# Kernel tuning notes

Hardware: AMD Instinct MI355X
Metric: run time of the kernel (lower is better)

Reference implementation:

```python
import jax, jax.numpy as jnp
import numpy as np

VOCAB, H, B, S = 30522, 768, 32, 512


def setup_inputs() -> dict:
    key = jax.random.key(0)
    ks = jax.random.split(key, 12)
    inp = {
        'hiddens': jax.random.normal(ks[0], (B, S, H), dtype=jnp.float32),
        'input_ids': jax.random.randint(ks[1], (B, S), 0, VOCAB, dtype=jnp.int32),
        'in_table': jax.random.bernoulli(ks[2], 0.5, (VOCAB,)),
        'table': jax.random.normal(ks[3], (VOCAB, H), dtype=jnp.float32) * 0.05,
        'W1m': jax.random.normal(ks[4], (512, H), dtype=jnp.float32) * 0.03,
        'b1m': jnp.zeros((512,), jnp.float32),
        'W2m': jax.random.normal(ks[5], (H, 512), dtype=jnp.float32) * 0.03,
        'b2m': jnp.zeros((H,), jnp.float32),
        'Wa1': jax.random.normal(ks[6], (100, H), dtype=jnp.float32) * 0.03,
        'ba1': jnp.zeros((100,), jnp.float32),
        'Wa2': jax.random.normal(ks[7], (1, 100), dtype=jnp.float32) * 0.1,
        'ba2': jnp.zeros((1,), jnp.float32),
        'Wl': jax.random.normal(ks[8], (3, 2 * H), dtype=jnp.float32) * 0.02,
        'bl': jnp.zeros((3,), jnp.float32),
    }
    return inp


def reference(hiddens, input_ids, in_table, table, W1m, b1m, W2m, b2m,
              Wa1, ba1, Wa2, ba2, Wl, bl):
    # --- vectorized replacement of the per-token dict lookup + MLP2 loops ---
    # gather knowledge vectors for every token: [B,S,768]
    know = table[input_ids]
    # MLP2 up to X2 (only X2 is used downstream): 768 -> 512 -> 768, relu twice
    x = jax.nn.relu(jnp.einsum('bsh,kh->bsk', know, W1m) + b1m)   # [B,S,512]
    fine = jax.nn.relu(jnp.einsum('bsk,hk->bsh', x, W2m) + b2m)   # [B,S,768]
    # membership mask; position 0 (CLS) is never looked up in the loop
    pos = jnp.arange(input_ids.shape[1])[None, :]                 # [1,S]
    mask = in_table[input_ids] & (pos > 0)                        # [B,S] bool
    m = mask[..., None].astype(hiddens.dtype)
    # wordhiddens: fine vector where token in table else zeros
    wordhiddens = fine * m                                        # [B,S,768]
    # --- StructuredSelfAttention over wordhiddens[:, 1:] ---
    wh = wordhiddens[:, 1:]                                       # [B,S-1,768]
    a = jnp.tanh(jnp.einsum('bsh,ah->bsa', wh, Wa1) + ba1)        # [B,S-1,100]
    a = jnp.einsum('bsa,oa->bso', a, Wa2) + ba2                   # [B,S-1,1]
    attn = jax.nn.softmax(a, axis=1)                              # softmax over seq
    sent = jnp.einsum('bso,bsh->boh', attn, wh)                   # [B,1,768]
    cls_knowledge = jnp.sum(sent, axis=1)                         # r=1, [B,768]
    # --- classifier head (method='ce'; dropout in eval mode = identity) ---
    cls_feats = jnp.concatenate([hiddens[:, 0, :], cls_knowledge], axis=1)  # [B,1536]
    predicts = cls_feats @ Wl.T + bl                              # [B,3]
    return predicts
```

## Files before the change

kernel.cpp:

```cpp
#include <hip/hip_runtime.h>
#include <stdint.h>
#include <math.h>

#define B_ 32
#define S_ 512
#define H_ 768
#define V_ 30522
#define M_ (B_*S_)
#define N1_ 512

typedef __attribute__((ext_vector_type(8))) short bf16x8;
typedef __attribute__((ext_vector_type(4))) float f32x4;

__device__ __forceinline__ float bf2f(unsigned short u){
  union { unsigned int u; float f; } c; c.u = ((unsigned int)u)<<16; return c.f;
}
__device__ __forceinline__ unsigned short f2bf(float f){
  union { float f; unsigned int u; } c; c.f=f;
  unsigned int u = c.u + 0x7FFFu + ((c.u>>16)&1u);
  return (unsigned short)(u>>16);
}
__device__ __forceinline__ bool tbl_get(const void* t, int id, int flag){
  if(flag==1) return ((const int*)t)[id]!=0;
  if(flag==2) return ((const unsigned int*)t)[id]!=0u;
  return ((const unsigned char*)t)[id]!=0;
}
__device__ __forceinline__ void gload_lds16(const void* g, void* l){
  __builtin_amdgcn_global_load_lds(
    (const __attribute__((address_space(1))) void*)g,
    (__attribute__((address_space(3))) void*)l, 16, 0, 0);
}

__global__ __launch_bounds__(256) void k_prep(const void* __restrict__ in_table,
  const int* __restrict__ ids,
  const float* __restrict__ W1, const float* __restrict__ W2,
  const float* __restrict__ Wa1, const float* __restrict__ Wa2, const float* __restrict__ ba1,
  unsigned short* __restrict__ W1bf, unsigned short* __restrict__ W2bf,
  unsigned short* __restrict__ Wa1bf, float* __restrict__ Wa2p, float* __restrict__ ba1p,
  int* __restrict__ cid, int* __restrict__ cnt)
{
  const int blk = blockIdx.x;
  const int t = threadIdx.x;
  if(blk < 32){
    __shared__ int sh[512];
    __shared__ int sflag;
    if(t < 64){
      const int v = ((const int*)in_table)[t];
      const unsigned int u = (unsigned int)v;
      const unsigned long long b01 = __ballot(v==0 || v==1);
      const unsigned long long bfl = __ballot(u==0u || u==0x3F800000u);
      if(t==0) sflag = (~b01==0ull) ? 1 : ((~bfl==0ull) ? 2 : 0);
    }
    __syncthreads();
    const int flag = sflag;
    const int m0 = blk*S_ + t, m1 = m0 + 256;
    const int id0 = ids[m0], id1 = ids[m1];
    const int mk0 = ((t!=0) && tbl_get(in_table, id0, flag)) ? 1 : 0;
    const int mk1 = tbl_get(in_table, id1, flag) ? 1 : 0;
    sh[t] = mk0; sh[t+256] = mk1;
    __syncthreads();
    for(int off=1; off<512; off<<=1){
      const int a0 = (t >= off) ? sh[t-off] : 0;
      const int a1 = (t+256 >= off) ? sh[t+256-off] : 0;
      __syncthreads();
      sh[t] += a0; sh[t+256] += a1;
      __syncthreads();
    }
    const int total = sh[511];
    const int r0 = sh[t] - mk0;
    const int r1 = sh[t+256] - mk1;
    if(t >= total)     cid[blk*S_ + t]       = 0;
    if(t+256 >= total) cid[blk*S_ + t + 256] = 0;
    if(mk0) cid[blk*S_ + r0] = id0;
    if(mk1) cid[blk*S_ + r1] = id1;
    if(t==0) cnt[blk] = total;
  } else {
    const int g = (blk-32)*256 + t, st = (gridDim.x-32)*256;
    for(int i=g;i<512*H_;i+=st) W1bf[i]=f2bf(W1[i]);
    for(int i=g;i<H_*512;i+=st) W2bf[i]=f2bf(W2[i]);
    for(int i=g;i<128*H_;i+=st) Wa1bf[i] = (i<100*H_)? f2bf(Wa1[i]) : (unsigned short)0;
    if(g < 128){ Wa2p[g] = (g<100)? Wa2[g] : 0.f; ba1p[g] = (g<100)? ba1[g] : 0.f; }
  }
}

__global__ __launch_bounds__(256) void k_gemm1g(
  const float* __restrict__ table, const int* __restrict__ cid,
  const unsigned short* __restrict__ Bw, const float* __restrict__ bias,
  const int* __restrict__ cnt, unsigned short* __restrict__ C)
{
  const int m0 = blockIdx.x << 7;
  if((m0 & (S_-1)) >= cnt[m0 >> 9]) return;
  __shared__ __align__(16) float AsF[128*32];
  __shared__ __align__(16) unsigned short Bs[128*32];
  const int tid = threadIdx.x;
  const int lane = tid & 63;
  const int wave = tid >> 6;
  const int wr = wave >> 1, wc = wave & 1;
  const int n0 = blockIdx.y << 7;

  const float* gaq[4];
  #pragma unroll
  for(int q=0;q<4;q++){
    const int s = q*256 + tid;
    const int row = s >> 3, ch = s & 7;
    const int sch = ch ^ (row & 7);
    gaq[q] = table + (size_t)cid[m0 + row]*H_ + (sch<<2);
  }
  const int f0 = tid, f1 = 256 + tid;
  const int r0 = f0 >> 2, s0 = ((f0 & 3) ^ ((f0 >> 3) & 3)) << 3;
  const int r1 = f1 >> 2, s1 = ((f1 & 3) ^ ((f1 >> 3) & 3)) << 3;
  const unsigned short* gb0 = Bw + (size_t)(n0 + r0)*H_ + s0;
  const unsigned short* gb1 = Bw + (size_t)(n0 + r1)*H_ + s1;

  f32x4 acc[4][4] = {};
  const int arow = (wr<<6) + (lane & 15);
  const int brow = (wc<<6) + (lane & 15);
  const int kg = lane >> 4;
  const int slb = ((kg ^ ((lane>>1)&3)) << 3);

  for(int k0 = 0; k0 < H_; k0 += 32){
    #pragma unroll
    for(int q=0;q<4;q++)
      gload_lds16(gaq[q] + k0, AsF + (q*256 + tid)*4);
    gload_lds16(gb0 + k0, Bs + (wave<<9));
    gload_lds16(gb1 + k0, Bs + 2048 + (wave<<9));
    __syncthreads();
    bf16x8 a[4], b[4];
    #pragma unroll
    for(int m=0;m<4;m++){
      const int R = arow + (m<<4);
      const int c1 = (2*kg) ^ (R&7), c2 = (2*kg+1) ^ (R&7);
      const f32x4 fa = *(const f32x4*)(AsF + R*32 + (c1<<2));
      const f32x4 fb = *(const f32x4*)(AsF + R*32 + (c2<<2));
      union { float f; unsigned int u; } z0,z1,z2,z3,z4,z5,z6,z7;
      z0.f=fa.x; z1.f=fa.y; z2.f=fa.z; z3.f=fa.w;
      z4.f=fb.x; z5.f=fb.y; z6.f=fb.z; z7.f=fb.w;
      union { unsigned int w[4]; bf16x8 v; } cv;
      cv.w[0] = (z1.u & 0xFFFF0000u) | (z0.u >> 16);
      cv.w[1] = (z3.u & 0xFFFF0000u) | (z2.u >> 16);
      cv.w[2] = (z5.u & 0xFFFF0000u) | (z4.u >> 16);
      cv.w[3] = (z7.u & 0xFFFF0000u) | (z6.u >> 16);
      a[m] = cv.v;
    }
    #pragma unroll
    for(int n=0;n<4;n++) b[n] = *(const bf16x8*)(Bs + (brow + (n<<4))*32 + slb);
    #pragma unroll
    for(int m=0;m<4;m++)
      #pragma unroll
      for(int n=0;n<4;n++)
        acc[m][n] = __builtin_amdgcn_mfma_f32_16x16x32_bf16(a[m], b[n], acc[m][n], 0,0,0);
    __syncthreads();
  }

  const int crow0 = (lane>>4) << 2;
  const int ccol  = lane & 15;
  float bia[4];
  #pragma unroll
  for(int n=0;n<4;n++) bia[n] = bias[n0 + (wc<<6) + (n<<4) + ccol];
  #pragma unroll
  for(int m=0;m<4;m++){
    const int gr0 = m0 + (wr<<6) + (m<<4) + crow0;
    #pragma unroll
    for(int j=0;j<4;j++){
      const size_t rbase = (size_t)(gr0 + j) * N1_;
      #pragma unroll
      for(int n=0;n<4;n++){
        float v = acc[m][n][j] + bia[n];
        v = fmaxf(v, 0.f);
        C[rbase + n0 + (wc<<6) + (n<<4) + ccol] = f2bf(v);
      }
    }
  }
}

template<int KTOT, int NTOT>
__global__ __launch_bounds__(256) void k_gemm(
  const unsigned short* __restrict__ A, const unsigned short* __restrict__ Bw,
  const float* __restrict__ bias, const int* __restrict__ cnt,
  unsigned short* __restrict__ C)
{
  const int m0 = blockIdx.x << 7;
  if((m0 & (S_-1)) >= cnt[m0 >> 9]) return;
  __shared__ __align__(16) unsigned short As[128*32];
  __shared__ __align__(16) unsigned short Bs[128*32];
  const int tid = threadIdx.x;
  const int lane = tid & 63;
  const int wave = tid >> 6;
  const int wr = wave >> 1, wc = wave & 1;
  const int n0 = blockIdx.y << 7;

  const int f0 = tid, f1 = 256 + tid;
  const int r0 = f0 >> 2, s0 = ((f0 & 3) ^ ((f0 >> 3) & 3)) << 3;
  const int r1 = f1 >> 2, s1 = ((f1 & 3) ^ ((f1 >> 3) & 3)) << 3;
  const unsigned short* ga0 = A + (size_t)(m0 + r0)*KTOT + s0;
  const unsigned short* ga1 = A + (size_t)(m0 + r1)*KTOT + s1;
  const unsigned short* gb0 = Bw + (size_t)(n0 + r0)*KTOT + s0;
  const unsigned short* gb1 = Bw + (size_t)(n0 + r1)*KTOT + s1;
  unsigned short* la0 = As + (wave<<9);
  unsigned short* la1 = As + 2048 + (wave<<9);
  unsigned short* lb0 = Bs + (wave<<9);
  unsigned short* lb1 = Bs + 2048 + (wave<<9);

  f32x4 acc[4][4] = {};
  const int arow = (wr<<6) + (lane & 15);
  const int brow = (wc<<6) + (lane & 15);
  const int sl   = (((lane>>4) ^ ((lane>>1)&3)) << 3);

  for(int k0 = 0; k0 < KTOT; k0 += 32){
    gload_lds16(ga0 + k0, la0);
    gload_lds16(ga1 + k0, la1);
    gload_lds16(gb0 + k0, lb0);
    gload_lds16(gb1 + k0, lb1);
    __syncthreads();
    bf16x8 a[4], b[4];
    #pragma unroll
    for(int m=0;m<4;m++) a[m] = *(const bf16x8*)(As + (arow + (m<<4))*32 + sl);
    #pragma unroll
    for(int n=0;n<4;n++) b[n] = *(const bf16x8*)(Bs + (brow + (n<<4))*32 + sl);
    #pragma unroll
    for(int m=0;m<4;m++)
      #pragma unroll
      for(int n=0;n<4;n++)
        acc[m][n] = __builtin_amdgcn_mfma_f32_16x16x32_bf16(a[m], b[n], acc[m][n], 0,0,0);
    __syncthreads();
  }

  const int crow0 = (lane>>4) << 2;
  const int ccol  = lane & 15;
  float bia[4];
  #pragma unroll
  for(int n=0;n<4;n++) bia[n] = bias[n0 + (wc<<6) + (n<<4) + ccol];
  #pragma unroll
  for(int m=0;m<4;m++){
    const int gr0 = m0 + (wr<<6) + (m<<4) + crow0;
    #pragma unroll
    for(int j=0;j<4;j++){
      const size_t rbase = (size_t)(gr0 + j) * NTOT;
      #pragma unroll
      for(int n=0;n<4;n++){
        float v = acc[m][n][j] + bia[n];
        v = fmaxf(v, 0.f);
        C[rbase + n0 + (wc<<6) + (n<<4) + ccol] = f2bf(v);
      }
    }
  }
}

__global__ __launch_bounds__(256) void k_score(
  const unsigned short* __restrict__ A, const unsigned short* __restrict__ Bw,
  const float* __restrict__ ba1p, const float* __restrict__ Wa2p, const float* __restrict__ ba2,
  const int* __restrict__ cnt, float* __restrict__ scoresC)
{
  const int m0 = blockIdx.x << 7;
  const int scnt = cnt[m0 >> 9];
  const int mbase = m0 & (S_-1);
  if(mbase >= scnt) return;
  __shared__ __align__(16) unsigned short As[128*32];
  __shared__ __align__(16) unsigned short Bs[128*32];
  __shared__ float sums[128][2];
  const int tid = threadIdx.x;
  const int lane = tid & 63;
  const int wave = tid >> 6;
  const int wr = wave >> 1, wc = wave & 1;

  const int f0 = tid, f1 = 256 + tid;
  const int r0 = f0 >> 2, s0 = ((f0 & 3) ^ ((f0 >> 3) & 3)) << 3;
  const int r1 = f1 >> 2, s1 = ((f1 & 3) ^ ((f1 >> 3) & 3)) << 3;
  const unsigned short* ga0 = A + (size_t)(m0 + r0)*H_ + s0;
  const unsigned short* ga1 = A + (size_t)(m0 + r1)*H_ + s1;
  const unsigned short* gb0 = Bw + (size_t)r0*H_ + s0;
  const unsigned short* gb1 = Bw + (size_t)r1*H_ + s1;
  unsigned short* la0 = As + (wave<<9);
  unsigned short* la1 = As + 2048 + (wave<<9);
  unsigned short* lb0 = Bs + (wave<<9);
  unsigned short* lb1 = Bs + 2048 + (wave<<9);

  f32x4 acc[4][4] = {};
  const int arow = (wr<<6) + (lane & 15);
  const int brow = (wc<<6) + (lane & 15);
  const int sl   = (((lane>>4) ^ ((lane>>1)&3)) << 3);

  for(int k0 = 0; k0 < H_; k0 += 32){
    gload_lds16(ga0 + k0, la0);
    gload_lds16(ga1 + k0, la1);
    gload_lds16(gb0 + k0, lb0);
    gload_lds16(gb1 + k0, lb1);
    __syncthreads();
    bf16x8 a[4], b[4];
    #pragma unroll
    for(int m=0;m<4;m++) a[m] = *(const bf16x8*)(As + (arow + (m<<4))*32 + sl);
    #pragma unroll
    for(int n=0;n<4;n++) b[n] = *(const bf16x8*)(Bs + (brow + (n<<4))*32 + sl);
    #pragma unroll
    for(int m=0;m<4;m++)
      #pragma unroll
      for(int n=0;n<4;n++)
        acc[m][n] = __builtin_amdgcn_mfma_f32_16x16x32_bf16(a[m], b[n], acc[m][n], 0,0,0);
    __syncthreads();
  }

  float psum[4][4] = {};
  #pragma unroll
  for(int n=0;n<4;n++){
    const int c = (wc<<6) + (n<<4) + (lane & 15);
    const float w2 = Wa2p[c], bb = ba1p[c];
    #pragma unroll
    for(int m=0;m<4;m++)
      #pragma unroll
      for(int j=0;j<4;j++)
        psum[m][j] = fmaf(tanhf(acc[m][n][j] + bb), w2, psum[m][j]);
  }
  #pragma unroll
  for(int msk=1; msk<16; msk<<=1)
    #pragma unroll
    for(int m=0;m<4;m++)
      #pragma unroll
      for(int j=0;j<4;j++)
        psum[m][j] += __shfl_xor(psum[m][j], msk, 64);
  if((lane & 15) == 0){
    #pragma unroll
    for(int m=0;m<4;m++)
      #pragma unroll
      for(int j=0;j<4;j++)
        sums[(wr<<6) + (m<<4) + ((lane>>4)<<2) + j][wc] = psum[m][j];
  }
  __syncthreads();
  if(tid < 128 && (mbase + tid) < scnt)
    scoresC[m0 + tid] = sums[tid][0] + sums[tid][1] + ba2[0];
}

__global__ __launch_bounds__(256) void k_partial(
  const float* __restrict__ scoresC, const int* __restrict__ cnt,
  const unsigned short* __restrict__ wh,
  const float* __restrict__ Wa2, const float* __restrict__ ba1, const float* __restrict__ ba2,
  float* __restrict__ partial)
{
  const int b = blockIdx.x >> 4, ch = blockIdx.x & 15, tid = threadIdx.x;
  const int n = cnt[b];
  const int j0 = ch << 5;
  const int nch = min(n - j0, 32);
  if(nch <= 0){
    if(tid < 192) *(float4*)(partial + (size_t)blockIdx.x*H_ + (tid<<2)) = float4{0.f,0.f,0.f,0.f};
    return;
  }
  __shared__ float red[256];
  __shared__ float sw[32];
  red[tid] = (tid < 100) ? Wa2[tid]*tanhf(ba1[tid]) : 0.f;
  __syncthreads();
  for(int st=128; st>0; st>>=1){ if(tid<st) red[tid]+=red[tid+st]; __syncthreads(); }
  const float c0 = red[0] + ba2[0];
  __syncthreads();
  const float s1 = (tid     < n) ? scoresC[b*S_ + tid      ] : -1e30f;
  const float s2 = (tid+256 < n) ? scoresC[b*S_ + tid + 256] : -1e30f;
  float lm = fmaxf(s1, s2);
  if(tid==0 && n < 511) lm = fmaxf(lm, c0);
  red[tid] = lm; __syncthreads();
  for(int st=128; st>0; st>>=1){ if(tid<st) red[tid]=fmaxf(red[tid], red[tid+st]); __syncthreads(); }
  const float mx = red[0]; __syncthreads();
  const float e1 = (tid     < n) ? __expf(s1-mx) : 0.f;
  const float e2 = (tid+256 < n) ? __expf(s2-mx) : 0.f;
  red[tid] = e1+e2; __syncthreads();
  for(int st=128; st>0; st>>=1){ if(tid<st) red[tid]+=red[tid+st]; __syncthreads(); }
  const float denom = red[0] + (float)(511 - n) * __expf(c0 - mx);
  const float inv = 1.f/denom;
  if(tid < 32){
    const int j = j0 + tid;
    sw[tid] = (j < n) ? __expf(scoresC[b*S_+j]-mx)*inv : 0.f;
  }
  __syncthreads();
  if(tid < 192){
    float a0=0.f, a1=0.f, a2=0.f, a3=0.f;
    const unsigned short* wp = wh + ((size_t)(b*S_ + j0))*H_ + (tid<<2);
    #pragma unroll 4
    for(int t=0;t<nch;t++){
      const float wv = sw[t];
      const ushort4 v = *(const ushort4*)(wp + (size_t)t*H_);
      a0 = fmaf(wv, bf2f(v.x), a0);
      a1 = fmaf(wv, bf2f(v.y), a1);
      a2 = fmaf(wv, bf2f(v.z), a2);
      a3 = fmaf(wv, bf2f(v.w), a3);
    }
    *(float4*)(partial + (size_t)blockIdx.x*H_ + (tid<<2)) = float4{a0,a1,a2,a3};
  }
}

__global__ __launch_bounds__(256) void k_predict(const float* __restrict__ hiddens,
  const float* __restrict__ partial, const float* __restrict__ Wl, const float* __restrict__ bl,
  float* __restrict__ out){
  __shared__ float ck[768];
  __shared__ float red[256];
  const int b = blockIdx.x, tid = threadIdx.x;
  #pragma unroll
  for(int r=0;r<3;r++){
    const int h = tid + (r<<8);
    float s=0.f;
    #pragma unroll 4
    for(int c=0;c<16;c++) s += partial[((size_t)((b<<4)+c))*H_ + h];
    ck[h]=s;
  }
  __syncthreads();
  const float* hid = hiddens + (size_t)b * S_ * H_;
  for(int c=0;c<3;c++){
    float p=0.f;
    #pragma unroll
    for(int r=0;r<3;r++){
      const int h = tid + (r<<8);
      p = fmaf(hid[h], Wl[c*1536 + h], p);
      p = fmaf(ck[h],  Wl[c*1536 + 768 + h], p);
    }
    red[tid]=p; __syncthreads();
    for(int st=128; st>0; st>>=1){ if(tid<st) red[tid]+=red[tid+st]; __syncthreads(); }
    if(tid==0) out[b*3+c] = red[0] + bl[c];
    __syncthreads();
  }
}

extern "C" void kernel_launch(void* const* d_in, const int* in_sizes, int n_in,
                              void* d_out, int out_size, void* d_ws, size_t ws_size,
                              hipStream_t stream)
{
  const float* hiddens = (const float*)d_in[0];
  const int*   ids     = (const int*)d_in[1];
  const void*  in_tab  = d_in[2];
  const float* table   = (const float*)d_in[3];
  const float* W1      = (const float*)d_in[4];
  const float* b1      = (const float*)d_in[5];
  const float* W2      = (const float*)d_in[6];
  const float* b2      = (const float*)d_in[7];
  const float* Wa1     = (const float*)d_in[8];
  const float* ba1     = (const float*)d_in[9];
  const float* Wa2     = (const float*)d_in[10];
  const float* ba2     = (const float*)d_in[11];
  const float* Wl      = (const float*)d_in[12];
  const float* bl      = (const float*)d_in[13];
  float* out = (float*)d_out;

  char* w = (char*)d_ws;
  unsigned short* wh    = (unsigned short*)w;
  unsigned short* x     = (unsigned short*)(w + 25165824);
  unsigned short* W1bf  = (unsigned short*)(w + 41943040);
  unsigned short* W2bf  = (unsigned short*)(w + 42729472);
  unsigned short* Wa1bf = (unsigned short*)(w + 43515904);
  float* Wa2p    = (float*)(w + 43712512);
  float* ba1p    = (float*)(w + 43713024);
  float* scoresC = (float*)(w + 43713536);
  int*   cid     = (int*)  (w + 43779072);
  int*   cnt     = (int*)  (w + 43844608);
  float* partial = (float*)(w + 43844736);

  hipLaunchKernelGGL(k_prep,   dim3(768), dim3(256), 0, stream, in_tab, ids,
                     W1, W2, Wa1, Wa2, ba1, W1bf, W2bf, Wa1bf, Wa2p, ba1p, cid, cnt);
  hipLaunchKernelGGL(k_gemm1g, dim3(128, 4), dim3(256), 0, stream, table, cid, W1bf, b1, cnt, x);
  hipLaunchKernelGGL((k_gemm<N1_, H_>), dim3(128, 6), dim3(256), 0, stream, x, W2bf, b2, cnt, wh);
  hipLaunchKernelGGL(k_score,   dim3(128), dim3(256), 0, stream, wh, Wa1bf, ba1p, Wa2p, ba2, cnt, scoresC);
  hipLaunchKernelGGL(k_partial, dim3(512), dim3(256), 0, stream, scoresC, cnt, wh, Wa2, ba1, ba2, partial);
  hipLaunchKernelGGL(k_predict, dim3(32),  dim3(256), 0, stream, hiddens, partial, Wl, bl, out);
}
```

Baseline: 90.62 us.

## Double-buffer LDS in GEMM kernels and shrink score tile to 32 rows

Adds double-buffered LDS staging to the gather-GEMM, the generic GEMM and the score kernel, so the next K-slice is loaded while MFMAs run on the current one. The score kernel is also retiled from 128-row to 32-row blocks with four waves splitting the 128 attention columns, which quadruples the grid to 512 blocks for better CU occupancy. The cost is doubled LDS per block, which may lower occupancy. Small tiles also reload the Wa1 weights more often.

```diff
diff --git a/kernel.cpp b/kernel.cpp
--- a/kernel.cpp
+++ b/kernel.cpp
@@ -90,8 +90,8 @@
 {
   const int m0 = blockIdx.x << 7;
   if((m0 & (S_-1)) >= cnt[m0 >> 9]) return;
-  __shared__ __align__(16) float AsF[128*32];
-  __shared__ __align__(16) unsigned short Bs[128*32];
+  __shared__ __align__(16) float AsF[2][128*32];
+  __shared__ __align__(16) unsigned short Bs[2][128*32];
   const int tid = threadIdx.x;
   const int lane = tid & 63;
   const int wave = tid >> 6;
@@ -118,20 +118,21 @@
   const int kg = lane >> 4;
   const int slb = ((kg ^ ((lane>>1)&3)) << 3);
 
-  for(int k0 = 0; k0 < H_; k0 += 32){
+  auto STAGE = [&](int buf, int k0){
     #pragma unroll
     for(int q=0;q<4;q++)
-      gload_lds16(gaq[q] + k0, AsF + (q*256 + tid)*4);
-    gload_lds16(gb0 + k0, Bs + (wave<<9));
-    gload_lds16(gb1 + k0, Bs + 2048 + (wave<<9));
-    __syncthreads();
+      gload_lds16(gaq[q] + k0, AsF[buf] + (q*256 + tid)*4);
+    gload_lds16(gb0 + k0, Bs[buf] + (wave<<9));
+    gload_lds16(gb1 + k0, Bs[buf] + 2048 + (wave<<9));
+  };
+  auto COMPUTE = [&](int buf){
     bf16x8 a[4], b[4];
     #pragma unroll
     for(int m=0;m<4;m++){
       const int R = arow + (m<<4);
       const int c1 = (2*kg) ^ (R&7), c2 = (2*kg+1) ^ (R&7);
-      const f32x4 fa = *(const f32x4*)(AsF + R*32 + (c1<<2));
-      const f32x4 fb = *(const f32x4*)(AsF + R*32 + (c2<<2));
+      const f32x4 fa = *(const f32x4*)(AsF[buf] + R*32 + (c1<<2));
+      const f32x4 fb = *(const f32x4*)(AsF[buf] + R*32 + (c2<<2));
       union { float f; unsigned int u; } z0,z1,z2,z3,z4,z5,z6,z7;
       z0.f=fa.x; z1.f=fa.y; z2.f=fa.z; z3.f=fa.w;
       z4.f=fb.x; z5.f=fb.y; z6.f=fb.z; z7.f=fb.w;
@@ -143,12 +144,22 @@
       a[m] = cv.v;
     }
     #pragma unroll
-    for(int n=0;n<4;n++) b[n] = *(const bf16x8*)(Bs + (brow + (n<<4))*32 + slb);
+    for(int n=0;n<4;n++) b[n] = *(const bf16x8*)(Bs[buf] + (brow + (n<<4))*32 + slb);
     #pragma unroll
     for(int m=0;m<4;m++)
       #pragma unroll
       for(int n=0;n<4;n++)
         acc[m][n] = __builtin_amdgcn_mfma_f32_16x16x32_bf16(a[m], b[n], acc[m][n], 0,0,0);
+  };
+
+  STAGE(0, 0);
+  __syncthreads();
+  for(int k0 = 0; k0 < H_; k0 += 64){
+    if(k0+32 < H_) STAGE(1, k0+32);
+    COMPUTE(0);
+    __syncthreads();
+    if(k0+64 < H_) STAGE(0, k0+64);
+    COMPUTE(1);
     __syncthreads();
   }
 
@@ -181,8 +192,8 @@
 {
   const int m0 = blockIdx.x << 7;
   if((m0 & (S_-1)) >= cnt[m0 >> 9]) return;
-  __shared__ __align__(16) unsigned short As[128*32];
-  __shared__ __align__(16) unsigned short Bs[128*32];
+  __shared__ __align__(16) unsigned short As[2][128*32];
+  __shared__ __align__(16) unsigned short Bs[2][128*32];
   const int tid = threadIdx.x;
   const int lane = tid & 63;
   const int wave = tid >> 6;
@@ -196,32 +207,39 @@
   const unsigned short* ga1 = A + (size_t)(m0 + r1)*KTOT + s1;
   const unsigned short* gb0 = Bw + (size_t)(n0 + r0)*KTOT + s0;
   const unsigned short* gb1 = Bw + (size_t)(n0 + r1)*KTOT + s1;
-  unsigned short* la0 = As + (wave<<9);
-  unsigned short* la1 = As + 2048 + (wave<<9);
-  unsigned short* lb0 = Bs + (wave<<9);
-  unsigned short* lb1 = Bs + 2048 + (wave<<9);
 
   f32x4 acc[4][4] = {};
   const int arow = (wr<<6) + (lane & 15);
   const int brow = (wc<<6) + (lane & 15);
   const int sl   = (((lane>>4) ^ ((lane>>1)&3)) << 3);
 
-  for(int k0 = 0; k0 < KTOT; k0 += 32){
-    gload_lds16(ga0 + k0, la0);
-    gload_lds16(ga1 + k0, la1);
-    gload_lds16(gb0 + k0, lb0);
-    gload_lds16(gb1 + k0, lb1);
-    __syncthreads();
+  auto STAGE = [&](int buf, int k0){
+    gload_lds16(ga0 + k0, As[buf] + (wave<<9));
+    gload_lds16(ga1 + k0, As[buf] + 2048 + (wave<<9));
+    gload_lds16(gb0 + k0, Bs[buf] + (wave<<9));
+    gload_lds16(gb1 + k0, Bs[buf] + 2048 + (wave<<9));
+  };
+  auto COMPUTE = [&](int buf){
     bf16x8 a[4], b[4];
     #pragma unroll
-    for(int m=0;m<4;m++) a[m] = *(const bf16x8*)(As + (arow + (m<<4))*32 + sl);
-    #pragma unroll
-    for(int n=0;n<4;n++) b[n] = *(const bf16x8*)(Bs + (brow + (n<<4))*32 + sl);
+    for(int m=0;m<4;m++) a[m] = *(const bf16x8*)(As[buf] + (arow + (m<<4))*32 + sl);
+    #pragma unroll
+    for(int n=0;n<4;n++) b[n] = *(const bf16x8*)(Bs[buf] + (brow + (n<<4))*32 + sl);
     #pragma unroll
     for(int m=0;m<4;m++)
       #pragma unroll
       for(int n=0;n<4;n++)
         acc[m][n] = __builtin_amdgcn_mfma_f32_16x16x32_bf16(a[m], b[n], acc[m][n], 0,0,0);
+  };
+
+  STAGE(0, 0);
+  __syncthreads();
+  for(int k0 = 0; k0 < KTOT; k0 += 64){
+    if(k0+32 < KTOT) STAGE(1, k0+32);
+    COMPUTE(0);
+    __syncthreads();
+    if(k0+64 < KTOT) STAGE(0, k0+64);
+    COMPUTE(1);
     __syncthreads();
   }
 
@@ -251,82 +269,83 @@
   const float* __restrict__ ba1p, const float* __restrict__ Wa2p, const float* __restrict__ ba2,
   const int* __restrict__ cnt, float* __restrict__ scoresC)
 {
-  const int m0 = blockIdx.x << 7;
-  const int scnt = cnt[m0 >> 9];
-  const int mbase = m0 & (S_-1);
-  if(mbase >= scnt) return;
-  __shared__ __align__(16) unsigned short As[128*32];
-  __shared__ __align__(16) unsigned short Bs[128*32];
-  __shared__ float sums[128][2];
+  const int m0 = blockIdx.x << 5;
+  if((m0 & (S_-1)) >= cnt[m0 >> 9]) return;
+  __shared__ __align__(16) unsigned short As[2][32*32];
+  __shared__ __align__(16) unsigned short Bs[2][128*32];
+  __shared__ float sums[32][4];
   const int tid = threadIdx.x;
   const int lane = tid & 63;
   const int wave = tid >> 6;
-  const int wr = wave >> 1, wc = wave & 1;
-
+
+  const int fa = tid, ra = fa >> 2, sa = ((fa & 3) ^ ((fa >> 3) & 3)) << 3;
+  const unsigned short* gaS = A + (size_t)(m0 + ra)*H_ + sa;
   const int f0 = tid, f1 = 256 + tid;
   const int r0 = f0 >> 2, s0 = ((f0 & 3) ^ ((f0 >> 3) & 3)) << 3;
   const int r1 = f1 >> 2, s1 = ((f1 & 3) ^ ((f1 >> 3) & 3)) << 3;
-  const unsigned short* ga0 = A + (size_t)(m0 + r0)*H_ + s0;
-  const unsigned short* ga1 = A + (size_t)(m0 + r1)*H_ + s1;
   const unsigned short* gb0 = Bw + (size_t)r0*H_ + s0;
   const unsigned short* gb1 = Bw + (size_t)r1*H_ + s1;
-  unsigned short* la0 = As + (wave<<9);
-  unsigned short* la1 = As + 2048 + (wave<<9);
-  unsigned short* lb0 = Bs + (wave<<9);
-  unsigned short* lb1 = Bs + 2048 + (wave<<9);
-
-  f32x4 acc[4][4] = {};
-  const int arow = (wr<<6) + (lane & 15);
-  const int brow = (wc<<6) + (lane & 15);
-  const int sl   = (((lane>>4) ^ ((lane>>1)&3)) << 3);
-
-  for(int k0 = 0; k0 < H_; k0 += 32){
-    gload_lds16(ga0 + k0, la0);
-    gload_lds16(ga1 + k0, la1);
-    gload_lds16(gb0 + k0, lb0);
-    gload_lds16(gb1 + k0, lb1);
-    __syncthreads();
-    bf16x8 a[4], b[4];
-    #pragma unroll
-    for(int m=0;m<4;m++) a[m] = *(const bf16x8*)(As + (arow + (m<<4))*32 + sl);
-    #pragma unroll
-    for(int n=0;n<4;n++) b[n] = *(const bf16x8*)(Bs + (brow + (n<<4))*32 + sl);
-    #pragma unroll
-    for(int m=0;m<4;m++)
-      #pragma unroll
-      for(int n=0;n<4;n++)
+
+  f32x4 acc[2][2] = {};
+  const int sl = (((lane>>4) ^ ((lane>>1)&3)) << 3);
+
+  auto STAGE = [&](int buf, int k0){
+    if(wave < 2) gload_lds16(gaS + k0, As[buf] + (wave<<9));
+    gload_lds16(gb0 + k0, Bs[buf] + (wave<<9));
+    gload_lds16(gb1 + k0, Bs[buf] + 2048 + (wave<<9));
+  };
+  auto COMPUTE = [&](int buf){
+    bf16x8 a[2], b[2];
+    #pragma unroll
+    for(int m=0;m<2;m++) a[m] = *(const bf16x8*)(As[buf] + ((lane&15) + (m<<4))*32 + sl);
+    #pragma unroll
+    for(int n=0;n<2;n++) b[n] = *(const bf16x8*)(Bs[buf] + ((wave<<5) + (n<<4) + (lane&15))*32 + sl);
+    #pragma unroll
+    for(int m=0;m<2;m++)
+      #pragma unroll
+      for(int n=0;n<2;n++)
         acc[m][n] = __builtin_amdgcn_mfma_f32_16x16x32_bf16(a[m], b[n], acc[m][n], 0,0,0);
-    __syncthreads();
-  }
-
-  float psum[4][4] = {};
-  #pragma unroll
-  for(int n=0;n<4;n++){
-    const int c = (wc<<6) + (n<<4) + (lane & 15);
+  };
+
+  STAGE(0, 0);
+  __syncthreads();
+  for(int k0 = 0; k0 < H_; k0 += 64){
+    if(k0+32 < H_) STAGE(1, k0+32);
+    COMPUTE(0);
+    __syncthreads();
+    if(k0+64 < H_) STAGE(0, k0+64);
+    COMPUTE(1);
+    __syncthreads();
+  }
+
+  float ps[2][4] = {{0.f,0.f,0.f,0.f},{0.f,0.f,0.f,0.f}};
+  #pragma unroll
+  for(int n=0;n<2;n++){
+    const int c = (wave<<5) + (n<<4) + (lane & 15);
     const float w2 = Wa2p[c], bb = ba1p[c];
     #pragma unroll
-    for(int m=0;m<4;m++)
+    for(int m=0;m<2;m++)
       #pragma unroll
       for(int j=0;j<4;j++)
-        psum[m][j] = fmaf(tanhf(acc[m][n][j] + bb), w2, psum[m][j]);
+        ps[m][j] = fmaf(tanhf(acc[m][n][j] + bb), w2, ps[m][j]);
   }
   #pragma unroll
   for(int msk=1; msk<16; msk<<=1)
     #pragma unroll
-    for(int m=0;m<4;m++)
+    for(int m=0;m<2;m++)
       #pragma unroll
       for(int j=0;j<4;j++)
-        psum[m][j] += __shfl_xor(psum[m][j], msk, 64);
+        ps[m][j] += __shfl_xor(ps[m][j], msk, 64);
   if((lane & 15) == 0){
     #pragma unroll
-    for(int m=0;m<4;m++)
+    for(int m=0;m<2;m++)
       #pragma unroll
       for(int j=0;j<4;j++)
-        sums[(wr<<6) + (m<<4) + ((lane>>4)<<2) + j][wc] = psum[m][j];
-  }
-  __syncthreads();
-  if(tid < 128 && (mbase + tid) < scnt)
-    scoresC[m0 + tid] = sums[tid][0] + sums[tid][1] + ba2[0];
+        sums[(m<<4) + ((lane>>4)<<2) + j][wave] = ps[m][j];
+  }
+  __syncthreads();
+  if(tid < 32)
+    scoresC[m0 + tid] = sums[tid][0] + sums[tid][1] + sums[tid][2] + sums[tid][3] + ba2[0];
 }
 
 __global__ __launch_bounds__(256) void k_partial(
@@ -452,7 +471,7 @@
                      W1, W2, Wa1, Wa2, ba1, W1bf, W2bf, Wa1bf, Wa2p, ba1p, cid, cnt);
   hipLaunchKernelGGL(k_gemm1g, dim3(128, 4), dim3(256), 0, stream, table, cid, W1bf, b1, cnt, x);
   hipLaunchKernelGGL((k_gemm<N1_, H_>), dim3(128, 6), dim3(256), 0, stream, x, W2bf, b2, cnt, wh);
-  hipLaunchKernelGGL(k_score,   dim3(128), dim3(256), 0, stream, wh, Wa1bf, ba1p, Wa2p, ba2, cnt, scoresC);
+  hipLaunchKernelGGL(k_score,   dim3(512), dim3(256), 0, stream, wh, Wa1bf, ba1p, Wa2p, ba2, cnt, scoresC);
   hipLaunchKernelGGL(k_partial, dim3(512), dim3(256), 0, stream, scoresC, cnt, wh, Wa2, ba1, ba2, partial);
   hipLaunchKernelGGL(k_predict, dim3(32),  dim3(256), 0, stream, hiddens, partial, Wl, bl, out);
 }
```

Result: faster. 81.90 us (-9.6%).
